# Kernel tuning notes

Measured on AMD Instinct MI355X. Metric: run time of the kernel, lower is better.

## Reference

```python
import jax, jax.numpy as jnp
import numpy as np

SR = 32000
N_FFT = 1024
HOP = 320
N_MELS = 128
PCEN_EPS = 1e-6
LN_EPS = 1e-6


def _hz_to_mel(f):
    return 2595.0 * np.log10(1.0 + f / 700.0)


def _mel_to_hz(m):
    return 700.0 * (10.0 ** (m / 2595.0) - 1.0)


def make_mel_fb():
    # HTK-scale triangular mel filterbank, [n_freqs, n_mels] (torchaudio default)
    n_freqs = N_FFT // 2 + 1
    mels = np.linspace(_hz_to_mel(0.0), _hz_to_mel(SR / 2.0), N_MELS + 2)
    f_pts = _mel_to_hz(mels)                       # [n_mels+2]
    all_freqs = np.linspace(0.0, SR / 2.0, n_freqs)
    f_diff = f_pts[1:] - f_pts[:-1]
    slopes = f_pts[None, :] - all_freqs[:, None]   # [n_freqs, n_mels+2]
    down = -slopes[:, :-2] / f_diff[:-1]
    up = slopes[:, 2:] / f_diff[1:]
    fb = np.maximum(0.0, np.minimum(down, up))
    return fb.astype(np.float32)


def setup_inputs() -> dict:
    key = jax.random.key(0)
    x = jax.random.normal(key, (16, 320000), dtype=jnp.float32)
    return {
        "x": x,
        "mel_fb": jnp.asarray(make_mel_fb()),
        "log_s": jnp.asarray(np.log(0.025), dtype=jnp.float32),
        "log_alpha": jnp.asarray(np.log(0.98), dtype=jnp.float32),
        "log_delta": jnp.asarray(np.log(2.0), dtype=jnp.float32),
        "log_r": jnp.asarray(np.log(0.5), dtype=jnp.float32),
    }


def reference(x, mel_fb, log_s, log_alpha, log_delta, log_r):
    B, T = x.shape
    pad = N_FFT // 2
    xp = jnp.pad(x, ((0, 0), (pad, pad)), mode="reflect")
    n_frames = 1 + (xp.shape[1] - N_FFT) // HOP           # = T//HOP + 1
    idx = jnp.arange(n_frames)[:, None] * HOP + jnp.arange(N_FFT)[None, :]
    frames = xp[:, idx]                                    # [B, F, N_FFT]
    # periodic Hann window (torch.hann_window default)
    win = 0.5 * (1.0 - jnp.cos(2.0 * jnp.pi * jnp.arange(N_FFT) / N_FFT))
    spec = jnp.fft.rfft(frames * win, axis=-1)             # [B, F, N_FFT//2+1]
    power = spec.real ** 2 + spec.imag ** 2                # power spectrogram
    E = jnp.einsum("bfk,km->bfm", power, mel_fb)           # [B, F, M] mel energies

    s = jnp.exp(log_s)
    alpha = jnp.exp(log_alpha)
    delta = jnp.exp(log_delta)
    r = jnp.exp(log_r)

    # Causal exponential smoother M(t) = (1-s) M(t-1) + s E(t), M init = first frame
    E_t = jnp.swapaxes(E, 0, 1)                            # [F, B, M]

    def step(m, e):
        m = (1.0 - s) * m + s * e
        return m, m

    _, M_t = jax.lax.scan(step, E_t[0], E_t)
    smooth = jnp.swapaxes(M_t, 0, 1)                       # [B, F, M]

    pcen = (E / (PCEN_EPS + smooth) ** alpha + delta) ** r - delta ** r

    # affine-free layer_norm over last dim (n_mels), eps=1e-6
    mu = jnp.mean(pcen, axis=-1, keepdims=True)
    var = jnp.var(pcen, axis=-1, keepdims=True)
    return (pcen - mu) / jnp.sqrt(var + LN_EPS)
```

## Files before the change

### kernel.cpp

```cpp
#include <hip/hip_runtime.h>
#include <math.h>

#define SRATE   32000
#define NFFT    1024
#define HOP     320
#define NBINS   513
#define NMELS   128
#define NFRAMES 1001
#define NB      16
#define TLEN    320000
#define PCEN_EPS 1e-6f
#define LN_EPS   1e-6f
#define MAXW     64

#define CL      16
#define NCHUNK  63

__device__ __forceinline__ int P(int i) { return i + (i >> 3); }
#define ZPAD 1152

__global__ __launch_bounds__(256) void k_prep(
    const float* __restrict__ fb, int* __restrict__ kmin, int* __restrict__ klen,
    float* __restrict__ wv, float* __restrict__ win, float2* __restrict__ twg)
{
    const int blk = blockIdx.x;
    const int tid = threadIdx.x;
    if (blk < NMELS) {
        const int m = blk;
        __shared__ int smin[4], smax[4];
        int lmin = 1 << 30, lmax = -1;
        for (int k = tid; k < NBINS; k += 256) {
            if (fb[k * NMELS + m] > 0.f) {
                if (k < lmin) lmin = k;
                if (k > lmax) lmax = k;
            }
        }
        #pragma unroll
        for (int off = 32; off; off >>= 1) {
            int om = __shfl_xor(lmin, off); if (om < lmin) lmin = om;
            int ox = __shfl_xor(lmax, off); if (ox > lmax) lmax = ox;
        }
        if ((tid & 63) == 0) { smin[tid >> 6] = lmin; smax[tid >> 6] = lmax; }
        __syncthreads();
        int k0 = min(min(smin[0], smin[1]), min(smin[2], smin[3]));
        int k1 = max(max(smax[0], smax[1]), max(smax[2], smax[3]));
        int L  = (k1 < 0) ? 0 : min(k1 - k0 + 1, MAXW);
        if (tid == 0) { kmin[m] = (k1 < 0) ? 0 : k0; klen[m] = L; }
        if (tid < L) wv[m * MAXW + tid] = fb[(k0 + tid) * NMELS + m];
    } else {
        const int i = (blk - NMELS) * 256 + tid;
        if (i < NFFT) {
            float sp = sinpif((float)i * (1.0f / (float)NFFT));
            win[i] = sp * sp;
        } else if (i < NFFT + 256) {
            int n = i - NFFT;
            float sn, cn;
            sincospif((float)n * (1.0f / 512.0f), &sn, &cn);
            twg[n] = make_float2(cn, -sn);
        }
    }
}

__global__ __launch_bounds__(256, 4) void k_melspec(
    const float* __restrict__ x,
    const int*   __restrict__ kmin,
    const int*   __restrict__ klen,
    const float* __restrict__ wv,
    const float* __restrict__ fb,
    const float* __restrict__ win_g,
    const float2* __restrict__ twg,
    float* __restrict__ E,
    int usePacked)
{
    __shared__ float2 zA[2][ZPAD], zB[2][ZPAD];
    __shared__ float2 tws[256];

    const int tid = threadIdx.x;
    const int g   = blockIdx.x;

    if (usePacked) {
        tws[tid] = twg[tid];
    } else {
        float sn, cn;
        sincospif((float)tid * (1.0f / 512.0f), &sn, &cn);
        tws[tid] = make_float2(cn, -sn);
    }

    const int i0 = tid * 4;
    #pragma unroll
    for (int u = 0; u < 2; ++u) {
        const int fa = 4 * g + 2 * u;
        const int fbr = fa + 1;
        const int ba = fa / NFRAMES,  ta = fa  - ba * NFRAMES;
        const int bb = fbr / NFRAMES, tb = fbr - bb * NFRAMES;
        const float* xa = x + (size_t)ba * TLEN;
        const float* xb = x + (size_t)bb * TLEN;
        const int basea = ta * HOP - (NFFT / 2);
        const int baseb = tb * HOP - (NFFT / 2);
        const bool safe = usePacked &&
                          basea >= 0 && baseb >= 0 &&
                          (basea + NFFT - 1 < TLEN) && (baseb + NFFT - 1 < TLEN);
        if (safe) {
            float4 v0 = *(const float4*)(xa + basea + i0);
            float4 v1 = *(const float4*)(xb + baseb + i0);
            float4 w  = *(const float4*)(win_g + i0);
            zA[u][P(i0 + 0)] = make_float2(v0.x * w.x, v1.x * w.x);
            zA[u][P(i0 + 1)] = make_float2(v0.y * w.y, v1.y * w.y);
            zA[u][P(i0 + 2)] = make_float2(v0.z * w.z, v1.z * w.z);
            zA[u][P(i0 + 3)] = make_float2(v0.w * w.w, v1.w * w.w);
        } else {
            #pragma unroll
            for (int q = 0; q < 4; ++q) {
                const int i = i0 + q;
                int j0 = basea + i;
                j0 = (j0 < 0) ? -j0 : ((j0 >= TLEN) ? (2 * TLEN - 2 - j0) : j0);
                int j1 = baseb + i;
                j1 = (j1 < 0) ? -j1 : ((j1 >= TLEN) ? (2 * TLEN - 2 - j1) : j1);
                float w;
                if (usePacked) w = win_g[i];
                else { float sp = sinpif((float)i * (1.0f / (float)NFFT)); w = sp * sp; }
                zA[u][P(i)] = make_float2(xa[j0] * w, xb[j1] * w);
            }
        }
    }
    __syncthreads();

    float2 (*zs)[ZPAD] = zA;
    float2 (*zd)[ZPAD] = zB;
    #pragma unroll
    for (int st = 0; st < 5; ++st) {
        const int mm = 1 << (2 * st);
        const int n  = tid & ~(mm - 1);
        const int o  = (n << 2) | (tid & (mm - 1));
        float2 w1 = tws[n];
        const float c1 = w1.x, s1 = w1.y;
        const float c2 = c1 * c1 - s1 * s1, s2 = 2.f * c1 * s1;
        const float c3 = c1 * c2 - s1 * s2, s3 = c1 * s2 + s1 * c2;
        #pragma unroll
        for (int u = 0; u < 2; ++u) {
            float2 a0 = zs[u][P(tid)];
            float2 a1 = zs[u][P(tid + 256)];
            float2 a2 = zs[u][P(tid + 512)];
            float2 a3 = zs[u][P(tid + 768)];
            float t0r = a0.x + a2.x, t0i = a0.y + a2.y;
            float t1r = a0.x - a2.x, t1i = a0.y - a2.y;
            float t2r = a1.x + a3.x, t2i = a1.y + a3.y;
            float t3r = a1.y - a3.y, t3i = a3.x - a1.x;
            float y1r = t1r + t3r, y1i = t1i + t3i;
            float y2r = t0r - t2r, y2i = t0i - t2i;
            float y3r = t1r - t3r, y3i = t1i - t3i;
            zd[u][P(o)]          = make_float2(t0r + t2r,            t0i + t2i);
            zd[u][P(o + mm)]     = make_float2(y1r * c1 - y1i * s1,  y1r * s1 + y1i * c1);
            zd[u][P(o + 2 * mm)] = make_float2(y2r * c2 - y2i * s2,  y2r * s2 + y2i * c2);
            zd[u][P(o + 3 * mm)] = make_float2(y3r * c3 - y3i * s3,  y3r * s3 + y3i * c3);
        }
        __syncthreads();
        float2 (*tp)[ZPAD] = zs; zs = zd; zd = tp;
    }

    {
        const int u  = tid >> 7;
        const int kk = tid & 127;
        for (int k = kk; k < NBINS; k += 128) {
            float2 Z  = zs[u][P(k)];
            const int kr = (NFFT - k) & (NFFT - 1);
            float2 Zr = zs[u][P(kr)];
            float x1r = Z.x + Zr.x, x1i = Z.y - Zr.y;
            float x2r = Z.y + Zr.y, x2i = Zr.x - Z.x;
            zd[u][P(k)] = make_float2(0.25f * (x1r * x1r + x1i * x1i),
                                      0.25f * (x2r * x2r + x2i * x2i));
        }
    }
    __syncthreads();

    {
        const int u = tid >> 7;
        const int m = tid & 127;
        const int fa = 4 * g + 2 * u;
        float acc0 = 0.f, acc1 = 0.f;
        if (usePacked) {
            const int k0 = kmin[m], L = klen[m];
            const float* w = wv + m * MAXW;
            for (int j = 0; j < L; ++j) {
                float2 pk = zd[u][P(k0 + j)];
                float ww = w[j];
                acc0 += pk.x * ww; acc1 += pk.y * ww;
            }
        } else {
            for (int k = 0; k < NBINS; ++k) {
                float2 pk = zd[u][P(k)];
                float ww = fb[k * NMELS + m];
                acc0 += pk.x * ww; acc1 += pk.y * ww;
            }
        }
        E[(size_t)fa * NMELS + m]       = acc0;
        E[(size_t)(fa + 1) * NMELS + m] = acc1;
    }
}

__global__ __launch_bounds__(256) void k_pcen_chunk(
    const float* __restrict__ E, float* __restrict__ Bws,
    float* __restrict__ E0ws, const float* __restrict__ p_ls)
{
    const int gid = blockIdx.x * blockDim.x + threadIdx.x;
    const int m = gid & (NMELS - 1);
    const int c = (gid >> 7) % NCHUNK;
    const int b = gid / (NMELS * NCHUNK);

    const float s = expf(p_ls[0]);
    const float a = 1.f - s;

    const int t0 = c * CL;
    const int L  = (t0 + CL <= NFRAMES) ? CL : (NFRAMES - t0);
    const float* col = E + (size_t)b * NFRAMES * NMELS + m;

    if (c == 0) E0ws[b * NMELS + m] = col[0];

    float Bacc;
    if (L == CL) {
        float e[CL];
        #pragma unroll
        for (int j = 0; j < CL; ++j)
            e[j] = col[(size_t)(t0 + j) * NMELS];
        float p0 = 0.f, p1 = 0.f, p2 = 0.f, p3 = 0.f;
        #pragma unroll
        for (int u = 0; u < 4; ++u) {
            p0 = a * p0 + s * e[u];
            p1 = a * p1 + s * e[4 + u];
            p2 = a * p2 + s * e[8 + u];
            p3 = a * p3 + s * e[12 + u];
        }
        const float a2 = a * a, a4 = a2 * a2, a8 = a4 * a4, a12 = a8 * a4;
        Bacc = a12 * p0 + a8 * p1 + a4 * p2 + p3;
    } else {
        Bacc = 0.f;
        for (int j = 0; j < L; ++j)
            Bacc = a * Bacc + s * col[(size_t)(t0 + j) * NMELS];
    }
    Bws[gid] = Bacc;
}

__global__ __launch_bounds__(128) void k_pcen_ln(
    float* __restrict__ E, const float* __restrict__ Bws,
    const float* __restrict__ E0ws,
    const float* __restrict__ p_ls, const float* __restrict__ p_la,
    const float* __restrict__ p_ld, const float* __restrict__ p_lr)
{
    __shared__ float sm[CL][NMELS];

    const int m   = threadIdx.x;
    const int blk = blockIdx.x;
    const int b   = blk / NCHUNK;
    const int c   = blk - b * NCHUNK;

    const float s     = expf(p_ls[0]);
    const float alpha = expf(p_la[0]);
    const float delta = expf(p_ld[0]);
    const float r     = expf(p_lr[0]);
    const float dr    = __powf(delta, r);
    const float a     = 1.f - s;
    const float a2 = a * a, a4 = a2 * a2, a8 = a4 * a4;
    const float a16 = a8 * a8;

    float M = E0ws[b * NMELS + m];
    const float* Bcol = Bws + (size_t)b * NCHUNK * NMELS + m;
    int cc = 0;
    for (; cc + 8 <= c; cc += 8) {
        float b0 = Bcol[(size_t)(cc + 0) * NMELS];
        float b1 = Bcol[(size_t)(cc + 1) * NMELS];
        float b2 = Bcol[(size_t)(cc + 2) * NMELS];
        float b3 = Bcol[(size_t)(cc + 3) * NMELS];
        float b4 = Bcol[(size_t)(cc + 4) * NMELS];
        float b5 = Bcol[(size_t)(cc + 5) * NMELS];
        float b6 = Bcol[(size_t)(cc + 6) * NMELS];
        float b7 = Bcol[(size_t)(cc + 7) * NMELS];
        M = a16 * M + b0; M = a16 * M + b1; M = a16 * M + b2; M = a16 * M + b3;
        M = a16 * M + b4; M = a16 * M + b5; M = a16 * M + b6; M = a16 * M + b7;
    }
    for (; cc < c; ++cc)
        M = a16 * M + Bcol[(size_t)cc * NMELS];

    const int t0 = c * CL;
    const int L  = (t0 + CL <= NFRAMES) ? CL : (NFRAMES - t0);
    const float* col = E + ((size_t)b * NFRAMES + t0) * NMELS + m;

    if (L == CL) {
        float e[CL];
        #pragma unroll
        for (int j = 0; j < CL; ++j)
            e[j] = col[(size_t)j * NMELS];
        #pragma unroll
        for (int j = 0; j < CL; ++j) {
            M = a * M + s * e[j];
            float den = __powf(PCEN_EPS + M, alpha);
            sm[j][m] = __powf(e[j] / den + delta, r) - dr;
        }
    } else {
        for (int j = 0; j < L; ++j) {
            float e = col[(size_t)j * NMELS];
            M = a * M + s * e;
            float den = __powf(PCEN_EPS + M, alpha);
            sm[j][m] = __powf(e / den + delta, r) - dr;
        }
    }
    __syncthreads();

    const int wid  = m >> 6;
    const int lane = m & 63;
    for (int row = wid; row < L; row += 2) {
        float v0 = sm[row][lane], v1 = sm[row][lane + 64];
        float sum = v0 + v1;
        float sq  = v0 * v0 + v1 * v1;
        #pragma unroll
        for (int off = 32; off; off >>= 1) {
            sum += __shfl_xor(sum, off);
            sq  += __shfl_xor(sq,  off);
        }
        float mu  = sum * (1.f / 128.f);
        float var = sq * (1.f / 128.f) - mu * mu;
        float inv = rsqrtf(var + LN_EPS);
        float* p = E + ((size_t)b * NFRAMES + t0 + row) * NMELS;
        p[lane]      = (v0 - mu) * inv;
        p[lane + 64] = (v1 - mu) * inv;
    }
}

__global__ __launch_bounds__(256) void k_pcen_serial(
    float* __restrict__ E,
    const float* __restrict__ p_ls, const float* __restrict__ p_la,
    const float* __restrict__ p_ld, const float* __restrict__ p_lr)
{
    const int gid = blockIdx.x * blockDim.x + threadIdx.x;
    const int b = gid >> 7;
    const int m = gid & 127;

    const float s     = expf(p_ls[0]);
    const float alpha = expf(p_la[0]);
    const float delta = expf(p_ld[0]);
    const float r     = expf(p_lr[0]);
    const float dr    = powf(delta, r);
    const float a     = 1.f - s;

    float* col = E + (size_t)b * NFRAMES * NMELS + m;
    float M = col[0];
    for (int t = 0; t < NFRAMES; ++t) {
        float e = col[(size_t)t * NMELS];
        M = a * M + s * e;
        float den = __powf(PCEN_EPS + M, alpha);
        float p   = __powf(e / den + delta, r) - dr;
        col[(size_t)t * NMELS] = p;
    }
}

__global__ __launch_bounds__(256) void k_ln(float* __restrict__ out) {
    const int wid  = threadIdx.x >> 6;
    const int lane = threadIdx.x & 63;
    const int row  = blockIdx.x * 4 + wid;
    float* p = out + (size_t)row * NMELS;
    float v0 = p[lane], v1 = p[lane + 64];
    float sum = v0 + v1;
    float sq  = v0 * v0 + v1 * v1;
    #pragma unroll
    for (int off = 32; off; off >>= 1) {
        sum += __shfl_xor(sum, off);
        sq  += __shfl_xor(sq,  off);
    }
    float mu  = sum * (1.f / 128.f);
    float var = sq * (1.f / 128.f) - mu * mu;
    float inv = rsqrtf(var + LN_EPS);
    p[lane]      = (v0 - mu) * inv;
    p[lane + 64] = (v1 - mu) * inv;
}

extern "C" void kernel_launch(void* const* d_in, const int* in_sizes, int n_in,
                              void* d_out, int out_size, void* d_ws, size_t ws_size,
                              hipStream_t stream) {
    const float* x   = (const float*)d_in[0];
    const float* fb  = (const float*)d_in[1];
    const float* lsp = (const float*)d_in[2];
    const float* lap = (const float*)d_in[3];
    const float* ldp = (const float*)d_in[4];
    const float* lrp = (const float*)d_in[5];
    float* out = (float*)d_out;

    const size_t packElems = 128 + 128 + 8192 + 1024 + 512;
    const size_t scanElems = (size_t)NB * NCHUNK * NMELS;
    const size_t needPack  = packElems * 4;
    const size_t needScan  = (packElems + scanElems + (size_t)NB * NMELS) * 4;

    int usePacked = (ws_size >= needPack) ? 1 : 0;
    int useScan   = (ws_size >= needScan) ? 1 : 0;

    int*    kmin = (int*)d_ws;
    int*    klen = kmin + NMELS;
    float*  wv   = (float*)(klen + NMELS);
    float*  win  = wv + (size_t)NMELS * MAXW;
    float2* twg  = (float2*)(win + NFFT);
    float*  Bws  = (float*)(twg + 256);
    float*  E0ws = Bws + scanElems;

    if (usePacked)
        k_prep<<<NMELS + 5, 256, 0, stream>>>(fb, kmin, klen, wv, win, twg);

    k_melspec<<<NB * NFRAMES / 4, 256, 0, stream>>>(
        x, kmin, klen, wv, fb, win, twg, out, usePacked);

    if (useScan) {
        const int nThread = NB * NCHUNK * NMELS;
        k_pcen_chunk<<<nThread / 256, 256, 0, stream>>>(out, Bws, E0ws, lsp);
        k_pcen_ln<<<NB * NCHUNK, 128, 0, stream>>>(out, Bws, E0ws, lsp, lap, ldp, lrp);
    } else {
        k_pcen_serial<<<(NB * NMELS) / 256, 256, 0, stream>>>(out, lsp, lap, ldp, lrp);
        k_ln<<<(NB * NFRAMES) / 4, 256, 0, stream>>>(out);
    }
}
```

Measured before the change: 77.69 us.

## Add dedicated chunk-prefix scan kernel and drop trivial twiddles in last FFT stage

Replaces the per-block redundant prefix recomputation in the PCEN+LayerNorm kernel with a separate scan kernel. That kernel computes each chunk's starting smoother state once per (batch, mel) and writes it to the workspace, so the final kernel only loads one value. This removes O(chunks²) reads but adds an extra launch and a tiny 8-block serial kernel. Separately, the final radix-4 FFT stage is specialized to skip its twiddle multiplications, which are all unity there.

Measured after the change: 78.07 us. About the same (+0.5%).

```diff
diff --git a/kernel.cpp b/kernel.cpp
--- a/kernel.cpp
+++ b/kernel.cpp
@@ -128,7 +128,7 @@
     float2 (*zs)[ZPAD] = zA;
     float2 (*zd)[ZPAD] = zB;
     #pragma unroll
-    for (int st = 0; st < 5; ++st) {
+    for (int st = 0; st < 4; ++st) {
         const int mm = 1 << (2 * st);
         const int n  = tid & ~(mm - 1);
         const int o  = (n << 2) | (tid & (mm - 1));
@@ -153,6 +153,27 @@
             zd[u][P(o + mm)]     = make_float2(y1r * c1 - y1i * s1,  y1r * s1 + y1i * c1);
             zd[u][P(o + 2 * mm)] = make_float2(y2r * c2 - y2i * s2,  y2r * s2 + y2i * c2);
             zd[u][P(o + 3 * mm)] = make_float2(y3r * c3 - y3i * s3,  y3r * s3 + y3i * c3);
+        }
+        __syncthreads();
+        float2 (*tp)[ZPAD] = zs; zs = zd; zd = tp;
+    }
+
+    {
+        const int o = tid;
+        #pragma unroll
+        for (int u = 0; u < 2; ++u) {
+            float2 a0 = zs[u][P(tid)];
+            float2 a1 = zs[u][P(tid + 256)];
+            float2 a2 = zs[u][P(tid + 512)];
+            float2 a3 = zs[u][P(tid + 768)];
+            float t0r = a0.x + a2.x, t0i = a0.y + a2.y;
+            float t1r = a0.x - a2.x, t1i = a0.y - a2.y;
+            float t2r = a1.x + a3.x, t2i = a1.y + a3.y;
+            float t3r = a1.y - a3.y, t3i = a3.x - a1.x;
+            zd[u][P(o)]       = make_float2(t0r + t2r, t0i + t2i);
+            zd[u][P(o + 256)] = make_float2(t1r + t3r, t1i + t3i);
+            zd[u][P(o + 512)] = make_float2(t0r - t2r, t0i - t2i);
+            zd[u][P(o + 768)] = make_float2(t1r - t3r, t1i - t3i);
         }
         __syncthreads();
         float2 (*tp)[ZPAD] = zs; zs = zd; zd = tp;
@@ -200,7 +221,7 @@
 
 __global__ __launch_bounds__(256) void k_pcen_chunk(
     const float* __restrict__ E, float* __restrict__ Bws,
-    float* __restrict__ E0ws, const float* __restrict__ p_ls)
+    const float* __restrict__ p_ls)
 {
     const int gid = blockIdx.x * blockDim.x + threadIdx.x;
     const int m = gid & (NMELS - 1);
@@ -213,8 +234,6 @@
     const int t0 = c * CL;
     const int L  = (t0 + CL <= NFRAMES) ? CL : (NFRAMES - t0);
     const float* col = E + (size_t)b * NFRAMES * NMELS + m;
-
-    if (c == 0) E0ws[b * NMELS + m] = col[0];
 
     float Bacc;
     if (L == CL) {
@@ -240,9 +259,49 @@
     Bws[gid] = Bacc;
 }
 
+__global__ __launch_bounds__(256) void k_pcen_scan(
+    const float* __restrict__ E, const float* __restrict__ Bws,
+    float* __restrict__ Mws, const float* __restrict__ p_ls)
+{
+    const int gid = blockIdx.x * blockDim.x + threadIdx.x;
+    const int m = gid & (NMELS - 1);
+    const int b = gid >> 7;
+
+    const float s = expf(p_ls[0]);
+    const float a = 1.f - s;
+    const float a2 = a * a, a4 = a2 * a2, a8 = a4 * a4;
+    const float a16 = a8 * a8;
+
+    float M = E[(size_t)b * NFRAMES * NMELS + m];
+    const size_t base = (size_t)b * NCHUNK * NMELS + m;
+    Mws[base] = M;
+    int c = 0;
+    for (; c + 8 <= NCHUNK - 1; c += 8) {
+        float b0 = Bws[base + (size_t)(c + 0) * NMELS];
+        float b1 = Bws[base + (size_t)(c + 1) * NMELS];
+        float b2 = Bws[base + (size_t)(c + 2) * NMELS];
+        float b3 = Bws[base + (size_t)(c + 3) * NMELS];
+        float b4 = Bws[base + (size_t)(c + 4) * NMELS];
+        float b5 = Bws[base + (size_t)(c + 5) * NMELS];
+        float b6 = Bws[base + (size_t)(c + 6) * NMELS];
+        float b7 = Bws[base + (size_t)(c + 7) * NMELS];
+        M = a16 * M + b0; Mws[base + (size_t)(c + 1) * NMELS] = M;
+        M = a16 * M + b1; Mws[base + (size_t)(c + 2) * NMELS] = M;
+        M = a16 * M + b2; Mws[base + (size_t)(c + 3) * NMELS] = M;
+        M = a16 * M + b3; Mws[base + (size_t)(c + 4) * NMELS] = M;
+        M = a16 * M + b4; Mws[base + (size_t)(c + 5) * NMELS] = M;
+        M = a16 * M + b5; Mws[base + (size_t)(c + 6) * NMELS] = M;
+        M = a16 * M + b6; Mws[base + (size_t)(c + 7) * NMELS] = M;
+        M = a16 * M + b7; Mws[base + (size_t)(c + 8) * NMELS] = M;
+    }
+    for (; c < NCHUNK - 1; ++c) {
+        M = a16 * M + Bws[base + (size_t)c * NMELS];
+        Mws[base + (size_t)(c + 1) * NMELS] = M;
+    }
+}
+
 __global__ __launch_bounds__(128) void k_pcen_ln(
-    float* __restrict__ E, const float* __restrict__ Bws,
-    const float* __restrict__ E0ws,
+    float* __restrict__ E, const float* __restrict__ Mws,
     const float* __restrict__ p_ls, const float* __restrict__ p_la,
     const float* __restrict__ p_ld, const float* __restrict__ p_lr)
 {
@@ -259,30 +318,12 @@
     const float r     = expf(p_lr[0]);
     const float dr    = __powf(delta, r);
     const float a     = 1.f - s;
-    const float a2 = a * a, a4 = a2 * a2, a8 = a4 * a4;
-    const float a16 = a8 * a8;
-
-    float M = E0ws[b * NMELS + m];
-    const float* Bcol = Bws + (size_t)b * NCHUNK * NMELS + m;
-    int cc = 0;
-    for (; cc + 8 <= c; cc += 8) {
-        float b0 = Bcol[(size_t)(cc + 0) * NMELS];
-        float b1 = Bcol[(size_t)(cc + 1) * NMELS];
-        float b2 = Bcol[(size_t)(cc + 2) * NMELS];
-        float b3 = Bcol[(size_t)(cc + 3) * NMELS];
-        float b4 = Bcol[(size_t)(cc + 4) * NMELS];
-        float b5 = Bcol[(size_t)(cc + 5) * NMELS];
-        float b6 = Bcol[(size_t)(cc + 6) * NMELS];
-        float b7 = Bcol[(size_t)(cc + 7) * NMELS];
-        M = a16 * M + b0; M = a16 * M + b1; M = a16 * M + b2; M = a16 * M + b3;
-        M = a16 * M + b4; M = a16 * M + b5; M = a16 * M + b6; M = a16 * M + b7;
-    }
-    for (; cc < c; ++cc)
-        M = a16 * M + Bcol[(size_t)cc * NMELS];
 
     const int t0 = c * CL;
     const int L  = (t0 + CL <= NFRAMES) ? CL : (NFRAMES - t0);
     const float* col = E + ((size_t)b * NFRAMES + t0) * NMELS + m;
+
+    float M = Mws[((size_t)b * NCHUNK + c) * NMELS + m];
 
     if (L == CL) {
         float e[CL];
@@ -386,7 +427,7 @@
     const size_t packElems = 128 + 128 + 8192 + 1024 + 512;
     const size_t scanElems = (size_t)NB * NCHUNK * NMELS;
     const size_t needPack  = packElems * 4;
-    const size_t needScan  = (packElems + scanElems + (size_t)NB * NMELS) * 4;
+    const size_t needScan  = (packElems + 2 * scanElems) * 4;
 
     int usePacked = (ws_size >= needPack) ? 1 : 0;
     int useScan   = (ws_size >= needScan) ? 1 : 0;
@@ -397,7 +438,7 @@
     float*  win  = wv + (size_t)NMELS * MAXW;
     float2* twg  = (float2*)(win + NFFT);
     float*  Bws  = (float*)(twg + 256);
-    float*  E0ws = Bws + scanElems;
+    float*  Mws  = Bws + scanElems;
 
     if (usePacked)
         k_prep<<<NMELS + 5, 256, 0, stream>>>(fb, kmin, klen, wv, win, twg);
@@ -407,8 +448,9 @@
 
     if (useScan) {
         const int nThread = NB * NCHUNK * NMELS;
-        k_pcen_chunk<<<nThread / 256, 256, 0, stream>>>(out, Bws, E0ws, lsp);
-        k_pcen_ln<<<NB * NCHUNK, 128, 0, stream>>>(out, Bws, E0ws, lsp, lap, ldp, lrp);
+        k_pcen_chunk<<<nThread / 256, 256, 0, stream>>>(out, Bws, lsp);
+        k_pcen_scan<<<(NB * NMELS) / 256, 256, 0, stream>>>(out, Bws, Mws, lsp);
+        k_pcen_ln<<<NB * NCHUNK, 128, 0, stream>>>(out, Mws, lsp, lap, ldp, lrp);
     } else {
         k_pcen_serial<<<(NB * NMELS) / 256, 256, 0, stream>>>(out, lsp, lap, ldp, lrp);
         k_ln<<<(NB * NFRAMES) / 4, 256, 0, stream>>>(out);
```
